# Optimization experiments

Measured on AMD Instinct MI355X. Metric: run time of the kernel, lower is better.

The kernel has to match this reference:

```python
import jax, jax.numpy as jnp
import numpy as np

SIZE = 64

def _init_linear(key, out_f, in_f, bias):
    k1, k2 = jax.random.split(key)
    bound = 1.0 / np.sqrt(in_f)
    W = jax.random.uniform(k1, (out_f, in_f), jnp.float32, -bound, bound)
    if bias:
        b = jax.random.uniform(k2, (out_f,), jnp.float32, -bound, bound)
        return W, b
    return W, None

def setup_inputs() -> dict:
    key = jax.random.key(0)
    ks = jax.random.split(key, 8)
    B, Lq, Lc = 16, 256, 256
    query = jax.random.normal(ks[0], (B, Lq, SIZE), jnp.float32)
    bank = jax.random.normal(ks[1], (B, Lc, SIZE), jnp.float32)
    mask = jnp.zeros((B, Lq, Lc), dtype=bool)
    Wq, _ = _init_linear(ks[2], SIZE, SIZE, False)          # linear_query (no bias)
    Wc, bc = _init_linear(ks[3], SIZE, SIZE, True)           # linear_context (bias)
    Ws, bs = _init_linear(ks[4], 1, SIZE, True)              # linear_score
    Woq, _ = _init_linear(ks[5], SIZE, SIZE, False)          # linear_out_query (no bias)
    Woc, boc = _init_linear(ks[6], SIZE, SIZE, True)         # linear_out_context (bias since mlp)
    return {"query": query, "bank": bank, "mask": mask,
            "Wq": Wq, "Wc": Wc, "bc": bc, "Ws": Ws, "bs": bs,
            "Woq": Woq, "Woc": Woc, "boc": boc}

def reference(query, bank, mask, Wq, Wc, bc, Ws, bs, Woq, Woc, boc):
    # MLP (additive) attention score: tanh(Wq q + Wc c + bc) projected to scalar
    sq = jnp.einsum('bqd,ed->bqe', query, Wq)                 # [B,Lq,D]
    sc = jnp.einsum('bcd,ed->bce', bank, Wc) + bc             # [B,Lc,D]
    h = jnp.tanh(sq[:, :, None, :] + sc[:, None, :, :])       # [B,Lq,Lc,D]
    score = jnp.einsum('bqcd,od->bqc', h, Ws) + bs[0]         # [B,Lq,Lc]
    score = jnp.where(mask, -jnp.inf, score)
    attn = jax.nn.softmax(score, axis=-1)                     # [B,Lq,Lc]
    context = jnp.einsum('bqc,bcd->bqd', attn, bank)          # [B,Lq,D]
    output = (jnp.einsum('bqd,ed->bqe', context, Woc) + boc
              + jnp.einsum('bqd,ed->bqe', query, Woq))
    return (output, attn)
```

## Files before the change

kernel.cpp:

```cpp
#include <hip/hip_runtime.h>
#include <math.h>

#define B  16
#define LQ 256
#define LC 256
#define D  64
#define QT 4
#define TS   2.88539008177793f
#define L2E  1.44269504088896f
#define PAD  72
#define INPAD 36
#define TPAD 33
#define CP4  264

__global__ __launch_bounds__(256) void proj_kernel(
    const float* __restrict__ query, const float* __restrict__ bank,
    const float* __restrict__ Wq, const float* __restrict__ Wc,
    const float* __restrict__ bc,
    const float* __restrict__ Woq, const float* __restrict__ Woc,
    const float* __restrict__ boc,
    float* __restrict__ esq, float* __restrict__ esct,
    float* __restrict__ oq, float* __restrict__ wb)
{
    int t  = threadIdx.x;
    int tp = blockIdx.x >> 7;
    int rb = blockIdx.x & 127;
    int bb_x = (rb & 7) + ((rb >> 6) << 3);
    int jj   = (rb >> 3) & 7;
    int r0 = bb_x * 256 + jj * 32;

    __shared__ __align__(16) float in_t[64 * INPAD];
    __shared__ __align__(16) float w_t [64 * PAD];
    __shared__ float tr[64 * TPAD];

    const float* src = (tp & 1) ? bank : query;
    const float* W   = (tp == 0) ? Wq : (tp == 1) ? Wc : (tp == 2) ? Woq : Woc;

    #pragma unroll
    for (int it = 0; it < 2; ++it) {
        int g = it * 256 + t;
        int kc4 = g & 15, row = g >> 4;
        float4 v = *reinterpret_cast<const float4*>(src + (r0 + row) * D + kc4 * 4);
        in_t[(kc4*4+0)*INPAD + row] = v.x; in_t[(kc4*4+1)*INPAD + row] = v.y;
        in_t[(kc4*4+2)*INPAD + row] = v.z; in_t[(kc4*4+3)*INPAD + row] = v.w;
    }
    #pragma unroll
    for (int it = 0; it < 4; ++it) {
        int g = it * 256 + t;
        int kc = (g >> 8) * 4 + (g & 3);
        int row = (g >> 2) & 63;
        float4 w = *reinterpret_cast<const float4*>(W + row * D + kc * 4);
        w_t[(kc*4+0)*PAD + row] = w.x; w_t[(kc*4+1)*PAD + row] = w.y;
        w_t[(kc*4+2)*PAD + row] = w.z; w_t[(kc*4+3)*PAD + row] = w.w;
    }
    __syncthreads();

    int cg = t & 15, rg = t >> 4;
    float acc[2][4];
    #pragma unroll
    for (int i = 0; i < 2; ++i)
        #pragma unroll
        for (int j = 0; j < 4; ++j) acc[i][j] = 0.f;

    #pragma unroll 8
    for (int k = 0; k < 64; ++k) {
        float2 a2 = *reinterpret_cast<const float2*>(&in_t[k * INPAD + rg * 2]);
        float4 w4 = *reinterpret_cast<const float4*>(&w_t [k * PAD + cg * 4]);
        acc[0][0]=fmaf(a2.x,w4.x,acc[0][0]); acc[0][1]=fmaf(a2.x,w4.y,acc[0][1]);
        acc[0][2]=fmaf(a2.x,w4.z,acc[0][2]); acc[0][3]=fmaf(a2.x,w4.w,acc[0][3]);
        acc[1][0]=fmaf(a2.y,w4.x,acc[1][0]); acc[1][1]=fmaf(a2.y,w4.y,acc[1][1]);
        acc[1][2]=fmaf(a2.y,w4.z,acc[1][2]); acc[1][3]=fmaf(a2.y,w4.w,acc[1][3]);
    }

    float4 b4 = {0.f, 0.f, 0.f, 0.f};
    if (tp == 1) b4 = *reinterpret_cast<const float4*>(bc  + cg * 4);
    if (tp == 3) b4 = *reinterpret_cast<const float4*>(boc + cg * 4);

    if (tp == 1) {
        #pragma unroll
        for (int i = 0; i < 2; ++i) {
            tr[(cg*4+0)*TPAD + rg*2+i] = exp2f(TS * (acc[i][0] + b4.x));
            tr[(cg*4+1)*TPAD + rg*2+i] = exp2f(TS * (acc[i][1] + b4.y));
            tr[(cg*4+2)*TPAD + rg*2+i] = exp2f(TS * (acc[i][2] + b4.z));
            tr[(cg*4+3)*TPAD + rg*2+i] = exp2f(TS * (acc[i][3] + b4.w));
        }
        __syncthreads();
        int bb = r0 >> 8;
        int cbase = r0 & 255;
        #pragma unroll
        for (int it = 0; it < 2; ++it) {
            int g = it * 256 + t;
            int d4 = g >> 5, cl = g & 31;
            float4 o;
            o.x = tr[(4*d4+0)*TPAD + cl];
            o.y = tr[(4*d4+1)*TPAD + cl];
            o.z = tr[(4*d4+2)*TPAD + cl];
            o.w = tr[(4*d4+3)*TPAD + cl];
            *reinterpret_cast<float4*>(esct + ((bb*16 + d4)*CP4 + cbase + cl)*4) = o;
        }
    } else {
        float* dst = (tp == 0) ? esq : (tp == 2) ? oq : wb;
        #pragma unroll
        for (int i = 0; i < 2; ++i) {
            float4 o;
            o.x = acc[i][0] + b4.x; o.y = acc[i][1] + b4.y;
            o.z = acc[i][2] + b4.z; o.w = acc[i][3] + b4.w;
            if (tp == 0) {
                o.x = exp2f(TS * o.x); o.y = exp2f(TS * o.y);
                o.z = exp2f(TS * o.z); o.w = exp2f(TS * o.w);
            }
            *reinterpret_cast<float4*>(dst + (r0 + rg*2 + i) * D + cg * 4) = o;
        }
    }
}

__global__ __launch_bounds__(256, 4) void attn_kernel(
    const unsigned char* __restrict__ mask,
    const float* __restrict__ esq_g, const float* __restrict__ esct_g,
    const float* __restrict__ Ws,
    const float* __restrict__ oq_g, const float* __restrict__ wb_g,
    float* __restrict__ out, float* __restrict__ attn_out)
{
    int t = threadIdx.x;
    int c = t;
    int p = blockIdx.x;
    int b = (p & 7) + ((p >> 9) << 3);
    int qb = (p >> 3) & 63;
    int bq0 = b * LQ + qb * QT;
    int lane = t & 63, wv = t >> 6;

    __shared__ __align__(16) float a_lds[QT][LC];
    __shared__ float part_lds[4 * QT * 64];
    __shared__ float red_s[4 * QT];

    const float* eqp = esq_g + bq0 * D;

    unsigned char mb[QT];
    #pragma unroll
    for (int qi = 0; qi < QT; ++qi) mb[qi] = mask[(bq0 + qi) * LC + c];

    const float4* ep4 = reinterpret_cast<const float4*>(esct_g) + b*16*CP4 + c;

    float s01[QT], s23[QT];
    #pragma unroll
    for (int qi = 0; qi < QT; ++qi) { s01[qi]=0.f; s23[qi]=0.f; }

    #pragma unroll
    for (int kb = 0; kb < 4; ++kb) {
        float4 ec4[4];
        #pragma unroll
        for (int j = 0; j < 4; ++j) ec4[j] = ep4[(kb*4 + j) * CP4];
        #pragma unroll
        for (int j = 0; j < 4; ++j) {
            const int d0 = kb * 16 + j * 4;
            float w0 = Ws[d0+0], w1 = Ws[d0+1];
            float w2 = Ws[d0+2], w3 = Ws[d0+3];
            #pragma unroll
            for (int qi = 0; qi < QT; ++qi) {
                float e0 = eqp[qi*D + d0+0];
                float e1 = eqp[qi*D + d0+1];
                float e2 = eqp[qi*D + d0+2];
                float e3 = eqp[qi*D + d0+3];
                float ax = fmaf(ec4[j].x, e0, 1.0f);
                float ay = fmaf(ec4[j].y, e1, 1.0f);
                float az = fmaf(ec4[j].z, e2, 1.0f);
                float aw = fmaf(ec4[j].w, e3, 1.0f);
                float nxy = fmaf(w0, ay, w1 * ax);
                float nzw = fmaf(w2, aw, w3 * az);
                s01[qi] = fmaf(nxy, __builtin_amdgcn_rcpf(ax * ay), s01[qi]);
                s23[qi] = fmaf(nzw, __builtin_amdgcn_rcpf(az * aw), s23[qi]);
            }
        }
    }

    float a[QT];
    #pragma unroll
    for (int qi = 0; qi < QT; ++qi) {
        a[qi] = mb[qi] ? 0.0f : exp2f(-TS * (s01[qi] + s23[qi]));
    }

    #pragma unroll
    for (int qi = 0; qi < QT; ++qi) {
        float ss = a[qi];
        #pragma unroll
        for (int o = 32; o > 0; o >>= 1) ss += __shfl_xor(ss, o);
        if (lane == 0) red_s[wv * QT + qi] = ss;
    }
    __syncthreads();
    #pragma unroll
    for (int qi = 0; qi < QT; ++qi) {
        float SUM = (red_s[qi] + red_s[QT + qi]) + (red_s[2*QT + qi] + red_s[3*QT + qi]);
        a[qi] *= __builtin_amdgcn_rcpf(SUM);
    }

    #pragma unroll
    for (int qi = 0; qi < QT; ++qi) {
        a_lds[qi][c] = a[qi];
        attn_out[(bq0 + qi) * LC + c] = a[qi];
    }
    __syncthreads();

    {
        int g = wv;
        float acc[QT];
        #pragma unroll
        for (int qi = 0; qi < QT; ++qi) acc[qi] = 0.f;
        const float* wbp = wb_g + (b * LC + g * 64) * D + lane;
        #pragma unroll
        for (int i0 = 0; i0 < 64; i0 += 4) {
            float4 A0 = *reinterpret_cast<const float4*>(&a_lds[0][g*64 + i0]);
            float4 A1 = *reinterpret_cast<const float4*>(&a_lds[1][g*64 + i0]);
            float4 A2 = *reinterpret_cast<const float4*>(&a_lds[2][g*64 + i0]);
            float4 A3 = *reinterpret_cast<const float4*>(&a_lds[3][g*64 + i0]);
            float w0 = wbp[(i0+0) * D];
            float w1 = wbp[(i0+1) * D];
            float w2 = wbp[(i0+2) * D];
            float w3 = wbp[(i0+3) * D];
            acc[0] = fmaf(A0.x, w0, acc[0]); acc[1] = fmaf(A1.x, w0, acc[1]);
            acc[2] = fmaf(A2.x, w0, acc[2]); acc[3] = fmaf(A3.x, w0, acc[3]);
            acc[0] = fmaf(A0.y, w1, acc[0]); acc[1] = fmaf(A1.y, w1, acc[1]);
            acc[2] = fmaf(A2.y, w1, acc[2]); acc[3] = fmaf(A3.y, w1, acc[3]);
            acc[0] = fmaf(A0.z, w2, acc[0]); acc[1] = fmaf(A1.z, w2, acc[1]);
            acc[2] = fmaf(A2.z, w2, acc[2]); acc[3] = fmaf(A3.z, w2, acc[3]);
            acc[0] = fmaf(A0.w, w3, acc[0]); acc[1] = fmaf(A1.w, w3, acc[1]);
            acc[2] = fmaf(A2.w, w3, acc[2]); acc[3] = fmaf(A3.w, w3, acc[3]);
        }
        #pragma unroll
        for (int qi = 0; qi < QT; ++qi)
            part_lds[(g * QT + qi) * 64 + lane] = acc[qi];
    }
    __syncthreads();

    {
        int qi = t >> 6, e = t & 63;
        float o = oq_g[bq0 * D + t];
        o += (part_lds[(0 * QT + qi) * 64 + e] + part_lds[(1 * QT + qi) * 64 + e])
           + (part_lds[(2 * QT + qi) * 64 + e] + part_lds[(3 * QT + qi) * 64 + e]);
        out[bq0 * D + t] = o;
    }
}

extern "C" void kernel_launch(void* const* d_in, const int* in_sizes, int n_in,
                              void* d_out, int out_size, void* d_ws, size_t ws_size,
                              hipStream_t stream) {
    const float* query = (const float*)d_in[0];
    const float* bank  = (const float*)d_in[1];
    const unsigned char* mask = (const unsigned char*)d_in[2];
    const float* Wq  = (const float*)d_in[3];
    const float* Wc  = (const float*)d_in[4];
    const float* bc  = (const float*)d_in[5];
    const float* Ws  = (const float*)d_in[6];
    const float* Woq = (const float*)d_in[8];
    const float* Woc = (const float*)d_in[9];
    const float* boc = (const float*)d_in[10];

    float* out  = (float*)d_out;
    float* attn = out + B * LQ * D;

    float* esq  = (float*)d_ws;
    float* esct = esq + B * LQ * D;
    float* oq   = esct + B * 16 * CP4 * 4;
    float* wb   = oq + B * LQ * D;

    proj_kernel<<<4 * 128, 256, 0, stream>>>(query, bank, Wq, Wc, bc,
                                             Woq, Woc, boc,
                                             esq, esct, oq, wb);
    attn_kernel<<<B * LQ / QT, 256, 0, stream>>>(mask, esq, esct, Ws,
                                                 oq, wb, out, attn);
}
```

Measured before the change: 26.91 us.

## Rewrite projection kernel to register-resident rows with wave-uniform scalar weights

The projection kernel no longer stages input and weight tiles through shared memory with transposes and barriers. Each thread now loads one full 64-wide input row into registers and computes 8 output features. The weight row index is made wave-uniform via readfirstlane, so weights can be fetched through scalar loads. This removes LDS traffic and syncs, at the cost of heavy register use (64 floats plus accumulators) and more redundant global reads of input rows across feature groups.

```diff
diff --git a/kernel.cpp b/kernel.cpp
--- a/kernel.cpp
+++ b/kernel.cpp
@@ -8,12 +8,9 @@
 #define QT 4
 #define TS   2.88539008177793f
 #define L2E  1.44269504088896f
-#define PAD  72
-#define INPAD 36
-#define TPAD 33
 #define CP4  264
 
-__global__ __launch_bounds__(256) void proj_kernel(
+__global__ __launch_bounds__(256, 2) void proj_kernel(
     const float* __restrict__ query, const float* __restrict__ bank,
     const float* __restrict__ Wq, const float* __restrict__ Wc,
     const float* __restrict__ bc,
@@ -22,95 +19,64 @@
     float* __restrict__ esq, float* __restrict__ esct,
     float* __restrict__ oq, float* __restrict__ wb)
 {
-    int t  = threadIdx.x;
-    int tp = blockIdx.x >> 7;
-    int rb = blockIdx.x & 127;
-    int bb_x = (rb & 7) + ((rb >> 6) << 3);
-    int jj   = (rb >> 3) & 7;
-    int r0 = bb_x * 256 + jj * 32;
-
-    __shared__ __align__(16) float in_t[64 * INPAD];
-    __shared__ __align__(16) float w_t [64 * PAD];
-    __shared__ float tr[64 * TPAD];
+    int t   = threadIdx.x;
+    int tp  = blockIdx.x >> 7;
+    int sub = blockIdx.x & 127;
+    int bbl = sub & 7, m = sub >> 3;
+    int bb  = bbl + ((m & 1) << 3);
+    int rc  = m >> 2;
+    int eh  = (m >> 1) & 1;
+    int lane = t & 63, wv = t >> 6;
+    int r = bb * 256 + rc * 64 + lane;
+    int ebase = __builtin_amdgcn_readfirstlane(eh * 32 + wv * 8);
 
     const float* src = (tp & 1) ? bank : query;
     const float* W   = (tp == 0) ? Wq : (tp == 1) ? Wc : (tp == 2) ? Woq : Woc;
 
-    #pragma unroll
-    for (int it = 0; it < 2; ++it) {
-        int g = it * 256 + t;
-        int kc4 = g & 15, row = g >> 4;
-        float4 v = *reinterpret_cast<const float4*>(src + (r0 + row) * D + kc4 * 4);
-        in_t[(kc4*4+0)*INPAD + row] = v.x; in_t[(kc4*4+1)*INPAD + row] = v.y;
-        in_t[(kc4*4+2)*INPAD + row] = v.z; in_t[(kc4*4+3)*INPAD + row] = v.w;
-    }
-    #pragma unroll
-    for (int it = 0; it < 4; ++it) {
-        int g = it * 256 + t;
-        int kc = (g >> 8) * 4 + (g & 3);
-        int row = (g >> 2) & 63;
-        float4 w = *reinterpret_cast<const float4*>(W + row * D + kc * 4);
-        w_t[(kc*4+0)*PAD + row] = w.x; w_t[(kc*4+1)*PAD + row] = w.y;
-        w_t[(kc*4+2)*PAD + row] = w.z; w_t[(kc*4+3)*PAD + row] = w.w;
-    }
-    __syncthreads();
-
-    int cg = t & 15, rg = t >> 4;
-    float acc[2][4];
-    #pragma unroll
-    for (int i = 0; i < 2; ++i)
-        #pragma unroll
-        for (int j = 0; j < 4; ++j) acc[i][j] = 0.f;
-
-    #pragma unroll 8
-    for (int k = 0; k < 64; ++k) {
-        float2 a2 = *reinterpret_cast<const float2*>(&in_t[k * INPAD + rg * 2]);
-        float4 w4 = *reinterpret_cast<const float4*>(&w_t [k * PAD + cg * 4]);
-        acc[0][0]=fmaf(a2.x,w4.x,acc[0][0]); acc[0][1]=fmaf(a2.x,w4.y,acc[0][1]);
-        acc[0][2]=fmaf(a2.x,w4.z,acc[0][2]); acc[0][3]=fmaf(a2.x,w4.w,acc[0][3]);
-        acc[1][0]=fmaf(a2.y,w4.x,acc[1][0]); acc[1][1]=fmaf(a2.y,w4.y,acc[1][1]);
-        acc[1][2]=fmaf(a2.y,w4.z,acc[1][2]); acc[1][3]=fmaf(a2.y,w4.w,acc[1][3]);
-    }
-
-    float4 b4 = {0.f, 0.f, 0.f, 0.f};
-    if (tp == 1) b4 = *reinterpret_cast<const float4*>(bc  + cg * 4);
-    if (tp == 3) b4 = *reinterpret_cast<const float4*>(boc + cg * 4);
+    float x[64];
+    const float4* rp = reinterpret_cast<const float4*>(src + r * D);
+    #pragma unroll
+    for (int i = 0; i < 16; ++i) {
+        float4 v = rp[i];
+        x[4*i+0] = v.x; x[4*i+1] = v.y; x[4*i+2] = v.z; x[4*i+3] = v.w;
+    }
+
+    const float* Wp = W + ebase * D;
+    float acc[8];
+    #pragma unroll
+    for (int e = 0; e < 8; ++e) acc[e] = 0.f;
+    #pragma unroll
+    for (int kc = 0; kc < 8; ++kc)
+        #pragma unroll
+        for (int e = 0; e < 8; ++e)
+            #pragma unroll
+            for (int kk = 0; kk < 8; ++kk)
+                acc[e] = fmaf(Wp[e * D + kc * 8 + kk], x[kc * 8 + kk], acc[e]);
 
     if (tp == 1) {
-        #pragma unroll
-        for (int i = 0; i < 2; ++i) {
-            tr[(cg*4+0)*TPAD + rg*2+i] = exp2f(TS * (acc[i][0] + b4.x));
-            tr[(cg*4+1)*TPAD + rg*2+i] = exp2f(TS * (acc[i][1] + b4.y));
-            tr[(cg*4+2)*TPAD + rg*2+i] = exp2f(TS * (acc[i][2] + b4.z));
-            tr[(cg*4+3)*TPAD + rg*2+i] = exp2f(TS * (acc[i][3] + b4.w));
-        }
-        __syncthreads();
-        int bb = r0 >> 8;
-        int cbase = r0 & 255;
-        #pragma unroll
-        for (int it = 0; it < 2; ++it) {
-            int g = it * 256 + t;
-            int d4 = g >> 5, cl = g & 31;
-            float4 o;
-            o.x = tr[(4*d4+0)*TPAD + cl];
-            o.y = tr[(4*d4+1)*TPAD + cl];
-            o.z = tr[(4*d4+2)*TPAD + cl];
-            o.w = tr[(4*d4+3)*TPAD + cl];
-            *reinterpret_cast<float4*>(esct + ((bb*16 + d4)*CP4 + cbase + cl)*4) = o;
-        }
+        int c = r & 255;
+        float v[8];
+        #pragma unroll
+        for (int e = 0; e < 8; ++e)
+            v[e] = exp2f(TS * (acc[e] + bc[ebase + e]));
+        int d4 = ebase >> 2;
+        float4 o0 = {v[0], v[1], v[2], v[3]};
+        float4 o1 = {v[4], v[5], v[6], v[7]};
+        *reinterpret_cast<float4*>(esct + ((bb*16 + d4    ) * CP4 + c) * 4) = o0;
+        *reinterpret_cast<float4*>(esct + ((bb*16 + d4 + 1) * CP4 + c) * 4) = o1;
     } else {
         float* dst = (tp == 0) ? esq : (tp == 2) ? oq : wb;
-        #pragma unroll
-        for (int i = 0; i < 2; ++i) {
-            float4 o;
-            o.x = acc[i][0] + b4.x; o.y = acc[i][1] + b4.y;
-            o.z = acc[i][2] + b4.z; o.w = acc[i][3] + b4.w;
-            if (tp == 0) {
-                o.x = exp2f(TS * o.x); o.y = exp2f(TS * o.y);
-                o.z = exp2f(TS * o.z); o.w = exp2f(TS * o.w);
-            }
-            *reinterpret_cast<float4*>(dst + (r0 + rg*2 + i) * D + cg * 4) = o;
+        float v[8];
+        #pragma unroll
+        for (int e = 0; e < 8; ++e) {
+            float a = acc[e];
+            if (tp == 3) a += boc[ebase + e];
+            v[e] = (tp == 0) ? exp2f(TS * a) : a;
         }
+        float4 o0 = {v[0], v[1], v[2], v[3]};
+        float4 o1 = {v[4], v[5], v[6], v[7]};
+        *reinterpret_cast<float4*>(dst + r * D + ebase    ) = o0;
+        *reinterpret_cast<float4*>(dst + r * D + ebase + 4) = o1;
     }
 }
 
```

Result: slower. 28.69 us (+6.6%).
